# Optimization experiments

Measured on AMD Instinct MI355X. Metric: run time of the kernel, lower is better.

The kernel has to match this reference:

```python
import jax, jax.numpy as jnp
import numpy as np

NUM_HEADS = 8


def _forward(x, Wq, bq, Wk, bk, Wv, bv, Wo, bo, w1, b1, w2, b2, tau):
    B, S, E = x.shape
    H = NUM_HEADS
    hd = E // H
    scale = hd ** -0.5

    def heads(t):
        return t.reshape(B, S, H, hd).transpose(0, 2, 1, 3)  # [B,H,S,hd]

    q = heads(x @ Wq + bq)
    k = heads(x @ Wk + bk)
    v = heads(x @ Wv + bv)
    s = jnp.einsum('bhqd,bhkd->bhqk', q, k) * scale  # [B,H,S,S]

    # ---- autopoietic transform (vectorized over batch, no mask) ----
    s = jnp.clip(jnp.nan_to_num(s, nan=0.0, posinf=10.0, neginf=-10.0), -15.0, 15.0)
    ma = s.mean(axis=1)  # mean over heads -> [B,S,S]
    eps_safe = 0.05  # clamp(eps=1e-6, 0.05, 0.8)
    sa = jnp.clip(jnp.clip(ma, -8.0, 8.0) * eps_safe, -10.0, 10.0)
    # 1x1 conv on [1,1,S,S] == per-channel scalar scale+bias -> [B,C,S,S]
    hid = jax.nn.relu(jnp.clip(sa[:, None] * w1[None, :, None, None]
                               + b1[None, :, None, None], -5.0, 5.0))
    ap = jnp.clip(jnp.einsum('bcij,c->bij', hid, w2) + b2, -5.0, 5.0)
    taylor = jnp.clip(1.0 + 0.05 * (ap * 50.0), 0.5, 1.5)
    sig = jax.nn.sigmoid(taylor)
    p = jax.nn.softmax(jnp.clip(ma, -10.0, 10.0), axis=-1)
    Hent = -p * jnp.log(p + 1e-6)
    Fm = jax.nn.softmax(3.0 * Hent, axis=-1)
    t = sig * Fm
    eo = jnp.sqrt((ma * ma).sum(axis=(1, 2), keepdims=True)) + 1e-4  # fro norm
    et = jnp.sqrt((t * t).sum(axis=(1, 2), keepdims=True)) + 1e-4
    t = jnp.clip(eo / et, 0.8, 1.2) * t
    tm = t.mean(axis=(1, 2), keepdims=True)
    om = ma.mean(axis=(1, 2), keepdims=True)
    tstd = jnp.sqrt(jnp.clip(((t - tm) ** 2).mean(axis=(1, 2), keepdims=True), 0.01, None))
    ostd = jnp.sqrt(jnp.clip(((ma - om) ** 2).mean(axis=(1, 2), keepdims=True), 0.01, None))
    gd = jnp.clip(ostd / tstd, 0.8, 1.2)
    ar = jnp.clip(jnp.abs(ma).max(axis=(1, 2), keepdims=True), 1.0, 10.0)
    sm = jnp.clip(0.3 / jnp.log1p(ar), 0.1, 0.5)
    st = tm + sm * gd * (t - tm)  # scaled_transform
    ent = Hent.mean(axis=(1, 2), keepdims=True)
    ne = ent / jnp.log(jnp.float32(S))  # normalized entropy (max_entropy = log S)
    rr = 0.4 * (1.0 - jnp.clip(ne, 0.0, 0.4))  # residual ratio (base 0.4, entropy-damped)
    # blend transform back into per-head scores (res_scale = 1.0)
    s = s + rr[:, None] * (st - ma)[:, None]

    attn = jax.nn.softmax(s / tau, axis=-1)
    out = jnp.einsum('bhqk,bhkd->bhqd', attn, v)
    out = out.transpose(0, 2, 1, 3).reshape(B, S, E)
    return out @ Wo + bo


def setup_inputs() -> dict:
    key = jax.random.key(0)
    ks = jax.random.split(key, 8)
    B, S, E, C = 4, 512, 512, 128
    w_scale = 0.02
    return {
        'x': jax.random.normal(ks[0], (B, S, E), dtype=jnp.float32),
        'Wq': jax.random.normal(ks[1], (E, E), dtype=jnp.float32) * w_scale,
        'bq': jnp.zeros((E,), jnp.float32),
        'Wk': jax.random.normal(ks[2], (E, E), dtype=jnp.float32) * w_scale,
        'bk': jnp.zeros((E,), jnp.float32),
        'Wv': jax.random.normal(ks[3], (E, E), dtype=jnp.float32) * w_scale,
        'bv': jnp.zeros((E,), jnp.float32),
        'Wo': jax.random.normal(ks[4], (E, E), dtype=jnp.float32) * w_scale,
        'bo': jnp.zeros((E,), jnp.float32),
        'w1': jax.random.normal(ks[5], (C,), dtype=jnp.float32) * 0.5,
        'b1': jnp.zeros((C,), jnp.float32),
        'w2': jax.random.normal(ks[6], (C,), dtype=jnp.float32) * 0.1,
        'b2': jnp.zeros((1,), jnp.float32),
        'tau': jnp.ones((1,), jnp.float32),
    }


def reference(x, Wq, bq, Wk, bk, Wv, bv, Wo, bo, w1, b1, w2, b2, tau):
    return _forward(x, Wq, bq, Wk, bk, Wv, bv, Wo, bo, w1, b1, w2, b2, tau)
```

## Files before the change

### kernel.cpp

```cpp
#include <hip/hip_runtime.h>
#include <math.h>

#define BB 4
#define SS 512
#define EE 512
#define NH 8
#define HD 64
#define NC 128
#define NTAB 4096

typedef _Float16 f16x8 __attribute__((ext_vector_type(8)));
typedef float f32x4 __attribute__((ext_vector_type(4)));

struct HL { _Float16 h, l; };

__device__ __forceinline__ float clampf(float v, float lo, float hi) {
  return fminf(fmaxf(v, lo), hi);
}
__device__ __forceinline__ HL split16(float x) {
  HL r;
  r.h = (_Float16)x;
  r.l = (_Float16)(x - (float)r.h);
  return r;
}

__device__ __forceinline__ float waveRedSum(float v) {
#pragma unroll
  for (int o = 32; o; o >>= 1) v += __shfl_xor(v, o);
  return v;
}
__device__ __forceinline__ float waveRedMax(float v) {
#pragma unroll
  for (int o = 32; o; o >>= 1) v = fmaxf(v, __shfl_xor(v, o));
  return v;
}
__device__ __forceinline__ float blockRedSum(float v, float* red) {
  int tid = threadIdx.x;
  v = waveRedSum(v);
  __syncthreads();
  if ((tid & 63) == 0) red[tid >> 6] = v;
  __syncthreads();
  return red[0] + red[1] + red[2] + red[3];
}
__device__ __forceinline__ float blockRedMax(float v, float* red) {
  int tid = threadIdx.x;
  v = waveRedMax(v);
  __syncthreads();
  if ((tid & 63) == 0) red[tid >> 6] = v;
  __syncthreads();
  return fmaxf(fmaxf(red[0], red[1]), fmaxf(red[2], red[3]));
}

__global__ __launch_bounds__(256) void k_prep(
    const float* __restrict__ w1, const float* __restrict__ b1,
    const float* __restrict__ w2, const float* __restrict__ b2,
    float* __restrict__ T, const float* __restrict__ x,
    _Float16* __restrict__ xh, _Float16* __restrict__ xl,
    const float* __restrict__ Wq, const float* __restrict__ Wk,
    const float* __restrict__ Wv, const float* __restrict__ Wo,
    _Float16* __restrict__ Wth, _Float16* __restrict__ Wtl) {
  const int bid = blockIdx.x;
  const int tid = threadIdx.x;
  if (bid < 17) {
    int idx = bid * 256 + tid;
    if (idx > NTAB) return;
    float sa = -0.4f + (float)idx * (0.8f / (float)NTAB);
    float ap = 0.f;
#pragma unroll 4
    for (int c = 0; c < NC; ++c) {
      float h = fminf(fmaxf(sa * w1[c] + b1[c], 0.f), 5.f);
      ap += h * w2[c];
    }
    ap = clampf(ap + b2[0], -5.f, 5.f);
    float tay = clampf(1.0f + 0.05f * (ap * 50.0f), 0.5f, 1.5f);
    T[idx] = 1.0f / (1.0f + expf(-tay));
  } else if (bid < 529) {
    int idx = ((bid - 17) * 256 + tid) * 8;
    float4 u0 = *(const float4*)(x + idx);
    float4 u1 = *(const float4*)(x + idx + 4);
    float f[8] = {u0.x, u0.y, u0.z, u0.w, u1.x, u1.y, u1.z, u1.w};
    f16x8 h, l;
#pragma unroll
    for (int j = 0; j < 8; ++j) {
      HL r = split16(f[j]);
      h[j] = r.h;
      l[j] = r.l;
    }
    *(f16x8*)(xh + idx) = h;
    *(f16x8*)(xl + idx) = l;
  } else {
    const int j = bid - 529;
    const int z = j >> 6;
    const int rem = j & 63;
    const int k0 = (rem & 7) * 64, n0 = (rem >> 3) * 64;
    const float* W = (z == 0) ? Wq : (z == 1) ? Wk : (z == 2) ? Wv : Wo;
    __shared__ float Tt[64][68];
    const int r = tid >> 2, c = (tid & 3) * 16;
#pragma unroll
    for (int jj = 0; jj < 16; jj += 4)
      *(float4*)&Tt[r][c + jj] =
          *(const float4*)(W + (size_t)(k0 + r) * EE + n0 + c + jj);
    __syncthreads();
    f16x8 h0, l0, h1, l1;
#pragma unroll
    for (int jj = 0; jj < 8; ++jj) {
      HL r0 = split16(Tt[c + jj][r]);
      HL r1 = split16(Tt[c + 8 + jj][r]);
      h0[jj] = r0.h; l0[jj] = r0.l;
      h1[jj] = r1.h; l1[jj] = r1.l;
    }
    _Float16* dh = Wth + ((size_t)z * EE + n0 + r) * EE + k0 + c;
    _Float16* dl = Wtl + ((size_t)z * EE + n0 + r) * EE + k0 + c;
    *(f16x8*)dh = h0;
    *(f16x8*)(dh + 8) = h1;
    *(f16x8*)dl = l0;
    *(f16x8*)(dl + 8) = l1;
  }
}

__global__ __launch_bounds__(256) void k_qkv_mfma(
    const _Float16* __restrict__ xh, const _Float16* __restrict__ xl,
    const _Float16* __restrict__ Wth, const _Float16* __restrict__ Wtl,
    const float* __restrict__ bq, const float* __restrict__ bk,
    const float* __restrict__ bv,
    _Float16* __restrict__ qh, _Float16* __restrict__ ql,
    _Float16* __restrict__ kh, _Float16* __restrict__ kl,
    _Float16* __restrict__ vth, _Float16* __restrict__ vtl) {
  const int which = blockIdx.z;
  const int tid = threadIdx.x;
  const int wave = tid >> 6, lane = tid & 63;
  const int quad = lane >> 4, l16 = lane & 15;
  const int m0 = blockIdx.y * 64;
  const int n0 = blockIdx.x * 64;
  const _Float16* Bh = Wth + (size_t)which * EE * EE;
  const _Float16* Bl = Wtl + (size_t)which * EE * EE;

  __shared__ __align__(16) char smpool[36864];
  _Float16(*LAh)[72] = (_Float16(*)[72])(smpool);
  _Float16(*LAl)[72] = (_Float16(*)[72])(smpool + 9216);
  _Float16(*LBh)[72] = (_Float16(*)[72])(smpool + 18432);
  _Float16(*LBl)[72] = (_Float16(*)[72])(smpool + 27648);
  float(*TR)[68] = (float(*)[68])(smpool);

  const int sr0 = tid >> 3, sc0 = (tid & 7) * 8;
  const int sr1 = sr0 + 32;

  f16x8 rA0h = *(const f16x8*)(xh + (size_t)(m0 + sr0) * EE + sc0);
  f16x8 rA0l = *(const f16x8*)(xl + (size_t)(m0 + sr0) * EE + sc0);
  f16x8 rB0h = *(const f16x8*)(Bh + (size_t)(n0 + sr0) * EE + sc0);
  f16x8 rB0l = *(const f16x8*)(Bl + (size_t)(n0 + sr0) * EE + sc0);
  f16x8 rA1h = *(const f16x8*)(xh + (size_t)(m0 + sr1) * EE + sc0);
  f16x8 rA1l = *(const f16x8*)(xl + (size_t)(m0 + sr1) * EE + sc0);
  f16x8 rB1h = *(const f16x8*)(Bh + (size_t)(n0 + sr1) * EE + sc0);
  f16x8 rB1l = *(const f16x8*)(Bl + (size_t)(n0 + sr1) * EE + sc0);

  f32x4 acc[4] = {};
  for (int k0 = 0; k0 < EE; k0 += 64) {
    if (k0) __syncthreads();
    *(f16x8*)&LAh[sr0][sc0] = rA0h;
    *(f16x8*)&LAl[sr0][sc0] = rA0l;
    *(f16x8*)&LBh[sr0][sc0] = rB0h;
    *(f16x8*)&LBl[sr0][sc0] = rB0l;
    *(f16x8*)&LAh[sr1][sc0] = rA1h;
    *(f16x8*)&LAl[sr1][sc0] = rA1l;
    *(f16x8*)&LBh[sr1][sc0] = rB1h;
    *(f16x8*)&LBl[sr1][sc0] = rB1l;
    __syncthreads();
    if (k0 + 64 < EE) {
      const int kn = k0 + 64;
      rA0h = *(const f16x8*)(xh + (size_t)(m0 + sr0) * EE + kn + sc0);
      rA0l = *(const f16x8*)(xl + (size_t)(m0 + sr0) * EE + kn + sc0);
      rB0h = *(const f16x8*)(Bh + (size_t)(n0 + sr0) * EE + kn + sc0);
      rB0l = *(const f16x8*)(Bl + (size_t)(n0 + sr0) * EE + kn + sc0);
      rA1h = *(const f16x8*)(xh + (size_t)(m0 + sr1) * EE + kn + sc0);
      rA1l = *(const f16x8*)(xl + (size_t)(m0 + sr1) * EE + kn + sc0);
      rB1h = *(const f16x8*)(Bh + (size_t)(n0 + sr1) * EE + kn + sc0);
      rB1l = *(const f16x8*)(Bl + (size_t)(n0 + sr1) * EE + kn + sc0);
    }
#pragma unroll
    for (int kk = 0; kk < 64; kk += 32) {
      f16x8 ah = *(const f16x8*)&LAh[wave * 16 + l16][kk + quad * 8];
      f16x8 al = *(const f16x8*)&LAl[wave * 16 + l16][kk + quad * 8];
#pragma unroll
      for (int nt = 0; nt < 4; ++nt) {
        f16x8 bhf = *(const f16x8*)&LBh[nt * 16 + l16][kk + quad * 8];
        f16x8 blf = *(const f16x8*)&LBl[nt * 16 + l16][kk + quad * 8];
        acc[nt] = __builtin_amdgcn_mfma_f32_16x16x32_f16(ah, bhf, acc[nt], 0, 0, 0);
        acc[nt] = __builtin_amdgcn_mfma_f32_16x16x32_f16(ah, blf, acc[nt], 0, 0, 0);
        acc[nt] = __builtin_amdgcn_mfma_f32_16x16x32_f16(al, bhf, acc[nt], 0, 0, 0);
      }
    }
  }
  const float* bias = (which == 0) ? bq : (which == 1) ? bk : bv;
  if (which == 2) {
    __syncthreads();
#pragma unroll
    for (int nt = 0; nt < 4; ++nt) {
      const int dcol = nt * 16 + l16;
      const float bb = bias[n0 + nt * 16 + l16];
#pragma unroll
      for (int r = 0; r < 4; ++r)
        TR[dcol][wave * 16 + quad * 4 + r] = acc[nt][r] + bb;
    }
    __syncthreads();
    const int d = tid >> 2, cc = (tid & 3) * 16;
    const int bh = (m0 >> 9) * NH + (n0 >> 6);
    const int si0 = m0 & 511;
    f16x8 h0, l0, h1, l1;
#pragma unroll
    for (int jj = 0; jj < 8; ++jj) {
      HL r0 = split16(TR[d][cc + jj]);
      HL r1 = split16(TR[d][cc + 8 + jj]);
      h0[jj] = r0.h; l0[jj] = r0.l;
      h1[jj] = r1.h; l1[jj] = r1.l;
    }
    _Float16* dh = vth + ((size_t)bh * HD + d) * SS + si0 + cc;
    _Float16* dl = vtl + ((size_t)bh * HD + d) * SS + si0 + cc;
    *(f16x8*)dh = h0;
    *(f16x8*)(dh + 8) = h1;
    *(f16x8*)dl = l0;
    *(f16x8*)(dl + 8) = l1;
  } else {
    const float postscale = (which == 0) ? 0.125f : 1.0f;
    const int mbase = m0 + wave * 16 + quad * 4;
#pragma unroll
    for (int nt = 0; nt < 4; ++nt) {
      const int col = n0 + nt * 16 + l16;
      const float bb = bias[col];
      const int hh = col >> 6, d = col & 63;
#pragma unroll
      for (int r = 0; r < 4; ++r) {
        const int mm = mbase + r;
        const int b_ = mm >> 9, si = mm & 511;
        const size_t idx = (((size_t)(b_ * NH + hh)) * SS + si) * HD + d;
        const float val = (acc[nt][r] + bb) * postscale;
        HL sp = split16(val);
        (which ? kh : qh)[idx] = sp.h;
        (which ? kl : ql)[idx] = sp.l;
      }
    }
  }
}

__global__ __launch_bounds__(256) void k_scores_mfma(
    const _Float16* __restrict__ qh, const _Float16* __restrict__ ql,
    const _Float16* __restrict__ kh, const _Float16* __restrict__ kl,
    float* __restrict__ s) {
  const int bh = blockIdx.z;
  const int i0 = blockIdx.y * 64, j0 = blockIdx.x * 64;
  const int tid = threadIdx.x;
  const int wave = tid >> 6, lane = tid & 63;
  const int quad = lane >> 4, l16 = lane & 15;

  __shared__ _Float16 Qh[64][72], Ql[64][72], Kh[64][72], Kl[64][72];
  const int r = tid >> 2, c = (tid & 3) * 16;
  {
    const size_t qoff = ((size_t)bh * SS + i0 + r) * HD + c;
    const size_t koff = ((size_t)bh * SS + j0 + r) * HD + c;
    *(f16x8*)&Qh[r][c] = *(const f16x8*)(qh + qoff);
    *(f16x8*)&Qh[r][c + 8] = *(const f16x8*)(qh + qoff + 8);
    *(f16x8*)&Ql[r][c] = *(const f16x8*)(ql + qoff);
    *(f16x8*)&Ql[r][c + 8] = *(const f16x8*)(ql + qoff + 8);
    *(f16x8*)&Kh[r][c] = *(const f16x8*)(kh + koff);
    *(f16x8*)&Kh[r][c + 8] = *(const f16x8*)(kh + koff + 8);
    *(f16x8*)&Kl[r][c] = *(const f16x8*)(kl + koff);
    *(f16x8*)&Kl[r][c + 8] = *(const f16x8*)(kl + koff + 8);
  }
  __syncthreads();

  f16x8 a_hi[2], a_lo[2];
#pragma unroll
  for (int ks = 0; ks < 2; ++ks) {
    a_hi[ks] = *(const f16x8*)&Qh[wave * 16 + l16][ks * 32 + quad * 8];
    a_lo[ks] = *(const f16x8*)&Ql[wave * 16 + l16][ks * 32 + quad * 8];
  }
  f32x4 acc[4] = {};
#pragma unroll
  for (int ks = 0; ks < 2; ++ks) {
#pragma unroll
    for (int t = 0; t < 4; ++t) {
      f16x8 b_hi = *(const f16x8*)&Kh[t * 16 + l16][ks * 32 + quad * 8];
      f16x8 b_lo = *(const f16x8*)&Kl[t * 16 + l16][ks * 32 + quad * 8];
      acc[t] = __builtin_amdgcn_mfma_f32_16x16x32_f16(a_hi[ks], b_hi,
                                                      acc[t], 0, 0, 0);
      acc[t] = __builtin_amdgcn_mfma_f32_16x16x32_f16(a_hi[ks], b_lo,
                                                      acc[t], 0, 0, 0);
      acc[t] = __builtin_amdgcn_mfma_f32_16x16x32_f16(a_lo[ks], b_hi,
                                                      acc[t], 0, 0, 0);
    }
  }
  float* sb = s + (size_t)bh * SS * SS;
#pragma unroll
  for (int t = 0; t < 4; ++t) {
#pragma unroll
    for (int r2 = 0; r2 < 4; ++r2) {
      float val = clampf(acc[t][r2], -15.0f, 15.0f);
      sb[(size_t)(i0 + wave * 16 + quad * 4 + r2) * SS + j0 + t * 16 + l16] = val;
    }
  }
}

__global__ __launch_bounds__(64) void k_rowstat(
    const float* __restrict__ s, const float* __restrict__ T,
    float* __restrict__ ma, float* __restrict__ t_un,
    float* __restrict__ rowred) {
  const int row = blockIdx.x;
  const int b_ = row >> 9, i = row & 511;
  const int lane = threadIdx.x;

  float4 a0 = {0.f, 0.f, 0.f, 0.f}, a1 = {0.f, 0.f, 0.f, 0.f};
#pragma unroll
  for (int hh = 0; hh < NH; ++hh) {
    const float4* p = reinterpret_cast<const float4*>(
                          s + (((size_t)(b_ * NH + hh) * SS) + i) * SS) +
                      lane * 2;
    float4 u0 = p[0], u1 = p[1];
    a0.x += u0.x; a0.y += u0.y; a0.z += u0.z; a0.w += u0.w;
    a1.x += u1.x; a1.y += u1.y; a1.z += u1.z; a1.w += u1.w;
  }
  float m[8] = {a0.x * 0.125f, a0.y * 0.125f, a0.z * 0.125f, a0.w * 0.125f,
                a1.x * 0.125f, a1.y * 0.125f, a1.z * 0.125f, a1.w * 0.125f};
  {
    float4* mp = reinterpret_cast<float4*>(ma + ((size_t)b_ * SS + i) * SS) +
                 lane * 2;
    float4 w0 = {m[0], m[1], m[2], m[3]}, w1v = {m[4], m[5], m[6], m[7]};
    mp[0] = w0;
    mp[1] = w1v;
  }
  float sma = 0.f, sma2 = 0.f, mabs = 0.f;
#pragma unroll
  for (int e = 0; e < 8; ++e) {
    sma += m[e];
    sma2 += m[e] * m[e];
    mabs = fmaxf(mabs, fabsf(m[e]));
  }
  sma = waveRedSum(sma);
  sma2 = waveRedSum(sma2);
  mabs = waveRedMax(mabs);

  float ex[8], esum = 0.f;
#pragma unroll
  for (int e = 0; e < 8; ++e) {
    ex[e] = expf(clampf(m[e], -10.f, 10.f));
    esum += ex[e];
  }
  esum = waveRedSum(esum);
  float inv = 1.0f / esum;
  float Hv[8], sH = 0.f;
#pragma unroll
  for (int e = 0; e < 8; ++e) {
    float p = ex[e] * inv;
    Hv[e] = -p * logf(p + 1e-6f);
    sH += Hv[e];
  }
  sH = waveRedSum(sH);

  float fx[8], fsum = 0.f;
#pragma unroll
  for (int e = 0; e < 8; ++e) {
    fx[e] = expf(3.0f * Hv[e]);
    fsum += fx[e];
  }
  fsum = waveRedSum(fsum);
  float finv = 1.0f / fsum;

  float t[8], st = 0.f, st2 = 0.f;
#pragma unroll
  for (int e = 0; e < 8; ++e) {
    float sa = clampf(m[e], -8.f, 8.f) * 0.05f;
    float pos = (sa + 0.4f) * ((float)NTAB / 0.8f);
    int idx = (int)pos;
    idx = idx < 0 ? 0 : (idx > NTAB - 1 ? NTAB - 1 : idx);
    float frac = pos - (float)idx;
    float g0 = T[idx], g1 = T[idx + 1];
    float sig = g0 + (g1 - g0) * frac;
    t[e] = sig * fx[e] * finv;
    st += t[e];
    st2 += t[e] * t[e];
  }
  st = waveRedSum(st);
  st2 = waveRedSum(st2);
  {
    float4* tp = reinterpret_cast<float4*>(t_un + ((size_t)b_ * SS + i) * SS) +
                 lane * 2;
    float4 w0 = {t[0], t[1], t[2], t[3]}, w1v = {t[4], t[5], t[6], t[7]};
    tp[0] = w0;
    tp[1] = w1v;
  }
  if (lane == 0) {
    float* rp = rowred + (size_t)row * 8;
    rp[0] = sma; rp[1] = sma2; rp[2] = mabs;
    rp[3] = st;  rp[4] = st2;  rp[5] = sH;
  }
}

__global__ __launch_bounds__(256) void k_consts(
    const float* __restrict__ rowred, float* __restrict__ cst) {
  const int b_ = blockIdx.x;
  const int tid = threadIdx.x;
  __shared__ float red[4];
  const float* r0 = rowred + ((size_t)b_ * SS + tid * 2) * 8;
  const float* r1 = r0 + 8;
  float sma = blockRedSum(r0[0] + r1[0], red);
  float sma2 = blockRedSum(r0[1] + r1[1], red);
  float mabs = blockRedMax(fmaxf(r0[2], r1[2]), red);
  float st = blockRedSum(r0[3] + r1[3], red);
  float st2 = blockRedSum(r0[4] + r1[4], red);
  float sH = blockRedSum(r0[5] + r1[5], red);
  if (tid == 0) {
    const float N = (float)(SS * SS);
    float eo = sqrtf(sma2) + 1e-4f;
    float et = sqrtf(st2) + 1e-4f;
    float r = clampf(eo / et, 0.8f, 1.2f);
    float tmean = r * st / N;
    float om = sma / N;
    float vart = r * r * fmaxf(st2 / N - (st / N) * (st / N), 0.f);
    float tstd = sqrtf(fmaxf(vart, 0.01f));
    float varo = fmaxf(sma2 / N - om * om, 0.f);
    float ostd = sqrtf(fmaxf(varo, 0.01f));
    float gd = clampf(ostd / tstd, 0.8f, 1.2f);
    float ar = clampf(mabs, 1.f, 10.f);
    float sm = clampf(0.3f / log1pf(ar), 0.1f, 0.5f);
    float ent = sH / N;
    float ne = ent / logf((float)SS);
    float rr = 0.4f * (1.f - clampf(ne, 0.f, 0.4f));
    float G = sm * gd;
    cst[b_ * 4 + 0] = rr * (1.f - G) * tmean;
    cst[b_ * 4 + 1] = rr * G * r;
    cst[b_ * 4 + 2] = rr;
  }
}

__global__ __launch_bounds__(256) void k_av_fused(
    const float* __restrict__ s, const float* __restrict__ ma,
    const float* __restrict__ t_un, const float* __restrict__ cst,
    const float* __restrict__ tau, const _Float16* __restrict__ vth,
    const _Float16* __restrict__ vtl, _Float16* __restrict__ oh,
    _Float16* __restrict__ ol) {
  const int bh = blockIdx.y;
  const int b_ = bh >> 3, hh = bh & 7;
  const int m0 = blockIdx.x * 32;
  const int tid = threadIdx.x;
  const int wave = tid >> 6, lane = tid & 63;
  const int quad = lane >> 4, l16 = lane & 15;

  const float c0 = cst[b_ * 4 + 0], c1 = cst[b_ * 4 + 1], c2 = cst[b_ * 4 + 2];
  const float itau = 1.0f / tau[0];

  __shared__ _Float16 Ph[32][40], Pl[32][40];
  __shared__ float Zp[32][4];

  const bool stager = (tid < 128);
  const int srow = tid >> 2;
  const int ci = tid & 3;
  const int schunk = ci * 8;
  const size_t sbase = ((size_t)bh * SS + m0 + (srow & 31)) * SS + schunk;
  const size_t mbase = ((size_t)b_ * SS + m0 + (srow & 31)) * SS + schunk;

  float4 sv0, sv1, mv0, mv1, tv0, tv1;
  if (stager) {
    sv0 = *(const float4*)(s + sbase);
    sv1 = *(const float4*)(s + sbase + 4);
    mv0 = *(const float4*)(ma + mbase);
    mv1 = *(const float4*)(ma + mbase + 4);
    tv0 = *(const float4*)(t_un + mbase);
    tv1 = *(const float4*)(t_un + mbase + 4);
  }

  float zpart = 0.f;
  f32x4 acc[2] = {};
  for (int k0 = 0; k0 < SS; k0 += 32) {
    if (k0) __syncthreads();
    if (stager) {
      float svv[8] = {sv0.x, sv0.y, sv0.z, sv0.w, sv1.x, sv1.y, sv1.z, sv1.w};
      float mvv[8] = {mv0.x, mv0.y, mv0.z, mv0.w, mv1.x, mv1.y, mv1.z, mv1.w};
      float tvv[8] = {tv0.x, tv0.y, tv0.z, tv0.w, tv1.x, tv1.y, tv1.z, tv1.w};
      f16x8 hv, lv;
#pragma unroll
      for (int j = 0; j < 8; ++j) {
        float vv = (svv[j] + c0 + c1 * tvv[j] - c2 * mvv[j]) * itau;
        float e = expf(vv) * 1.52587890625e-05f;
        zpart += e;
        HL r = split16(e);
        hv[j] = r.h;
        lv[j] = r.l;
      }
      *(f16x8*)&Ph[srow][schunk] = hv;
      *(f16x8*)&Pl[srow][schunk] = lv;
    }
    __syncthreads();
    if (stager && k0 + 32 < SS) {
      sv0 = *(const float4*)(s + sbase + k0 + 32);
      sv1 = *(const float4*)(s + sbase + k0 + 36);
      mv0 = *(const float4*)(ma + mbase + k0 + 32);
      mv1 = *(const float4*)(ma + mbase + k0 + 36);
      tv0 = *(const float4*)(t_un + mbase + k0 + 32);
      tv1 = *(const float4*)(t_un + mbase + k0 + 36);
    }
    const size_t boff = ((size_t)bh * HD + wave * 16 + l16) * SS + k0 + quad * 8;
    f16x8 bh_ = *(const f16x8*)(vth + boff);
    f16x8 bl_ = *(const f16x8*)(vtl + boff);
#pragma unroll
    for (int mt = 0; mt < 2; ++mt) {
      f16x8 ah = *(const f16x8*)&Ph[mt * 16 + l16][quad * 8];
      f16x8 al = *(const f16x8*)&Pl[mt * 16 + l16][quad * 8];
      acc[mt] = __builtin_amdgcn_mfma_f32_16x16x32_f16(ah, bh_, acc[mt], 0, 0, 0);
      acc[mt] = __builtin_amdgcn_mfma_f32_16x16x32_f16(ah, bl_, acc[mt], 0, 0, 0);
      acc[mt] = __builtin_amdgcn_mfma_f32_16x16x32_f16(al, bh_, acc[mt], 0, 0, 0);
    }
  }
  __syncthreads();
  if (stager) Zp[srow][ci] = zpart;
  __syncthreads();
#pragma unroll
  for (int mt = 0; mt < 2; ++mt) {
#pragma unroll
    for (int r = 0; r < 4; ++r) {
      const int lr = mt * 16 + quad * 4 + r;
      const float Z = Zp[lr][0] + Zp[lr][1] + Zp[lr][2] + Zp[lr][3];
      const float oV = acc[mt][r] / Z;
      const int si = m0 + lr;
      const size_t idx =
          ((size_t)(b_ * SS + si)) * EE + hh * HD + wave * 16 + l16;
      HL sp = split16(oV);
      oh[idx] = sp.h;
      ol[idx] = sp.l;
    }
  }
}

__global__ __launch_bounds__(256) void k_out_mfma(
    const _Float16* __restrict__ oh, const _Float16* __restrict__ ol,
    const _Float16* __restrict__ Wth, const _Float16* __restrict__ Wtl,
    const float* __restrict__ bo, float* __restrict__ out) {
  const int tid = threadIdx.x;
  const int wave = tid >> 6, lane = tid & 63;
  const int quad = lane >> 4, l16 = lane & 15;
  const int m0 = blockIdx.y * 64;
  const int n0 = blockIdx.x * 64;
  const _Float16* Bh = Wth + (size_t)3 * EE * EE;
  const _Float16* Bl = Wtl + (size_t)3 * EE * EE;

  __shared__ _Float16 LAh[64][72], LAl[64][72], LBh[64][72], LBl[64][72];

  const int sr0 = tid >> 3, sc0 = (tid & 7) * 8;
  const int sr1 = sr0 + 32;

  f16x8 rA0h = *(const f16x8*)(oh + (size_t)(m0 + sr0) * EE + sc0);
  f16x8 rA0l = *(const f16x8*)(ol + (size_t)(m0 + sr0) * EE + sc0);
  f16x8 rB0h = *(const f16x8*)(Bh + (size_t)(n0 + sr0) * EE + sc0);
  f16x8 rB0l = *(const f16x8*)(Bl + (size_t)(n0 + sr0) * EE + sc0);
  f16x8 rA1h = *(const f16x8*)(oh + (size_t)(m0 + sr1) * EE + sc0);
  f16x8 rA1l = *(const f16x8*)(ol + (size_t)(m0 + sr1) * EE + sc0);
  f16x8 rB1h = *(const f16x8*)(Bh + (size_t)(n0 + sr1) * EE + sc0);
  f16x8 rB1l = *(const f16x8*)(Bl + (size_t)(n0 + sr1) * EE + sc0);

  f32x4 acc[4] = {};
  for (int k0 = 0; k0 < EE; k0 += 64) {
    if (k0) __syncthreads();
    *(f16x8*)&LAh[sr0][sc0] = rA0h;
    *(f16x8*)&LAl[sr0][sc0] = rA0l;
    *(f16x8*)&LBh[sr0][sc0] = rB0h;
    *(f16x8*)&LBl[sr0][sc0] = rB0l;
    *(f16x8*)&LAh[sr1][sc0] = rA1h;
    *(f16x8*)&LAl[sr1][sc0] = rA1l;
    *(f16x8*)&LBh[sr1][sc0] = rB1h;
    *(f16x8*)&LBl[sr1][sc0] = rB1l;
    __syncthreads();
    if (k0 + 64 < EE) {
      const int kn = k0 + 64;
      rA0h = *(const f16x8*)(oh + (size_t)(m0 + sr0) * EE + kn + sc0);
      rA0l = *(const f16x8*)(ol + (size_t)(m0 + sr0) * EE + kn + sc0);
      rB0h = *(const f16x8*)(Bh + (size_t)(n0 + sr0) * EE + kn + sc0);
      rB0l = *(const f16x8*)(Bl + (size_t)(n0 + sr0) * EE + kn + sc0);
      rA1h = *(const f16x8*)(oh + (size_t)(m0 + sr1) * EE + kn + sc0);
      rA1l = *(const f16x8*)(ol + (size_t)(m0 + sr1) * EE + kn + sc0);
      rB1h = *(const f16x8*)(Bh + (size_t)(n0 + sr1) * EE + kn + sc0);
      rB1l = *(const f16x8*)(Bl + (size_t)(n0 + sr1) * EE + kn + sc0);
    }
#pragma unroll
    for (int kk = 0; kk < 64; kk += 32) {
      f16x8 ah = *(const f16x8*)&LAh[wave * 16 + l16][kk + quad * 8];
      f16x8 al = *(const f16x8*)&LAl[wave * 16 + l16][kk + quad * 8];
#pragma unroll
      for (int nt = 0; nt < 4; ++nt) {
        f16x8 bhf = *(const f16x8*)&LBh[nt * 16 + l16][kk + quad * 8];
        f16x8 blf = *(const f16x8*)&LBl[nt * 16 + l16][kk + quad * 8];
        acc[nt] = __builtin_amdgcn_mfma_f32_16x16x32_f16(ah, bhf, acc[nt], 0, 0, 0);
        acc[nt] = __builtin_amdgcn_mfma_f32_16x16x32_f16(ah, blf, acc[nt], 0, 0, 0);
        acc[nt] = __builtin_amdgcn_mfma_f32_16x16x32_f16(al, bhf, acc[nt], 0, 0, 0);
      }
    }
  }
  const int mbase = m0 + wave * 16 + quad * 4;
#pragma unroll
  for (int nt = 0; nt < 4; ++nt) {
    const int col = n0 + nt * 16 + l16;
    const float bb = bo[col];
#pragma unroll
    for (int r = 0; r < 4; ++r) {
      const int m = mbase + r;
      out[(size_t)m * EE + col] = acc[nt][r] + bb;
    }
  }
}

extern "C" void kernel_launch(void* const* d_in, const int* in_sizes, int n_in,
                              void* d_out, int out_size, void* d_ws,
                              size_t ws_size, hipStream_t stream) {
  const float* x = (const float*)d_in[0];
  const float* Wq = (const float*)d_in[1];
  const float* bq = (const float*)d_in[2];
  const float* Wk = (const float*)d_in[3];
  const float* bk = (const float*)d_in[4];
  const float* Wv = (const float*)d_in[5];
  const float* bv = (const float*)d_in[6];
  const float* Wo = (const float*)d_in[7];
  const float* bo = (const float*)d_in[8];
  const float* w1 = (const float*)d_in[9];
  const float* b1 = (const float*)d_in[10];
  const float* w2 = (const float*)d_in[11];
  const float* b2 = (const float*)d_in[12];
  const float* tau = (const float*)d_in[13];
  float* out = (float*)d_out;

  const size_t NX = (size_t)2048 * EE;
  const size_t NW = (size_t)4 * EE * EE;
  const size_t NQK = (size_t)BB * NH * SS * HD;
  const size_t NS = (size_t)BB * NH * SS * SS;

  _Float16* xh = (_Float16*)d_ws;
  _Float16* xl = xh + NX;
  _Float16* Wth = xl + NX;
  _Float16* Wtl = Wth + NW;
  _Float16* qh = Wtl + NW;
  _Float16* ql = qh + NQK;
  _Float16* kh = ql + NQK;
  _Float16* kl = kh + NQK;
  _Float16* vth = kl + NQK;
  _Float16* vtl = vth + NQK;
  float* s = (float*)(vtl + NQK);
  float* ma = s + NS;
  float* t_un = ma + (size_t)BB * SS * SS;
  float* T = t_un + (size_t)BB * SS * SS;
  float* rowred = T + 8192;
  float* cst = rowred + 2048 * 8;
  _Float16* oh = xh;
  _Float16* ol = xl;

  k_prep<<<785, 256, 0, stream>>>(w1, b1, w2, b2, T, x, xh, xl, Wq, Wk, Wv, Wo,
                                  Wth, Wtl);
  k_qkv_mfma<<<dim3(8, 32, 3), 256, 0, stream>>>(xh, xl, Wth, Wtl, bq, bk, bv,
                                                 qh, ql, kh, kl, vth, vtl);
  k_scores_mfma<<<dim3(8, 8, 32), 256, 0, stream>>>(qh, ql, kh, kl, s);
  k_rowstat<<<2048, 64, 0, stream>>>(s, T, ma, t_un, rowred);
  k_consts<<<4, 256, 0, stream>>>(rowred, cst);
  k_av_fused<<<dim3(16, 32), 256, 0, stream>>>(s, ma, t_un, cst, tau, vth, vtl,
                                               oh, ol);
  k_out_mfma<<<dim3(8, 32), 256, 0, stream>>>(oh, ol, Wth, Wtl, bo, out);
}
```

Before: 167.4 us.

## Fuse x split into QKV GEMM and replace consts kernel with atomics

The QKV GEMM now reads fp32 x directly and splits it into high/low fp16 halves in registers, so the separate conversion pass and its workspace round trip are gone. Per-row statistics are accumulated per batch with global atomics, and every av block derives the constants itself, which removes the k_consts launch. k_rowstat packs four rows into each 256-thread block. The costs are redundant splitting of x across the N-tile blocks, atomic contention, and a float atomicMax done on the uint bit pattern, which is valid only because mabs is non-negative.

Measured after the change: 276.5 us. 65.1% more time.

```diff
diff --git a/kernel.cpp b/kernel.cpp
--- a/kernel.cpp
+++ b/kernel.cpp
@@ -34,31 +34,15 @@
   for (int o = 32; o; o >>= 1) v = fmaxf(v, __shfl_xor(v, o));
   return v;
 }
-__device__ __forceinline__ float blockRedSum(float v, float* red) {
-  int tid = threadIdx.x;
-  v = waveRedSum(v);
-  __syncthreads();
-  if ((tid & 63) == 0) red[tid >> 6] = v;
-  __syncthreads();
-  return red[0] + red[1] + red[2] + red[3];
-}
-__device__ __forceinline__ float blockRedMax(float v, float* red) {
-  int tid = threadIdx.x;
-  v = waveRedMax(v);
-  __syncthreads();
-  if ((tid & 63) == 0) red[tid >> 6] = v;
-  __syncthreads();
-  return fmaxf(fmaxf(red[0], red[1]), fmaxf(red[2], red[3]));
-}
 
 __global__ __launch_bounds__(256) void k_prep(
     const float* __restrict__ w1, const float* __restrict__ b1,
     const float* __restrict__ w2, const float* __restrict__ b2,
-    float* __restrict__ T, const float* __restrict__ x,
-    _Float16* __restrict__ xh, _Float16* __restrict__ xl,
+    float* __restrict__ T,
     const float* __restrict__ Wq, const float* __restrict__ Wk,
     const float* __restrict__ Wv, const float* __restrict__ Wo,
-    _Float16* __restrict__ Wth, _Float16* __restrict__ Wtl) {
+    _Float16* __restrict__ Wth, _Float16* __restrict__ Wtl,
+    float* __restrict__ acc) {
   const int bid = blockIdx.x;
   const int tid = threadIdx.x;
   if (bid < 17) {
@@ -74,22 +58,8 @@
     ap = clampf(ap + b2[0], -5.f, 5.f);
     float tay = clampf(1.0f + 0.05f * (ap * 50.0f), 0.5f, 1.5f);
     T[idx] = 1.0f / (1.0f + expf(-tay));
-  } else if (bid < 529) {
-    int idx = ((bid - 17) * 256 + tid) * 8;
-    float4 u0 = *(const float4*)(x + idx);
-    float4 u1 = *(const float4*)(x + idx + 4);
-    float f[8] = {u0.x, u0.y, u0.z, u0.w, u1.x, u1.y, u1.z, u1.w};
-    f16x8 h, l;
-#pragma unroll
-    for (int j = 0; j < 8; ++j) {
-      HL r = split16(f[j]);
-      h[j] = r.h;
-      l[j] = r.l;
-    }
-    *(f16x8*)(xh + idx) = h;
-    *(f16x8*)(xl + idx) = l;
-  } else {
-    const int j = bid - 529;
+  } else if (bid < 273) {
+    const int j = bid - 17;
     const int z = j >> 6;
     const int rem = j & 63;
     const int k0 = (rem & 7) * 64, n0 = (rem >> 3) * 64;
@@ -115,11 +85,13 @@
     *(f16x8*)(dh + 8) = h1;
     *(f16x8*)dl = l0;
     *(f16x8*)(dl + 8) = l1;
+  } else {
+    if (tid < 32) acc[tid] = 0.0f;
   }
 }
 
 __global__ __launch_bounds__(256) void k_qkv_mfma(
-    const _Float16* __restrict__ xh, const _Float16* __restrict__ xl,
+    const float* __restrict__ x,
     const _Float16* __restrict__ Wth, const _Float16* __restrict__ Wtl,
     const float* __restrict__ bq, const float* __restrict__ bk,
     const float* __restrict__ bv,
@@ -145,35 +117,49 @@
   const int sr0 = tid >> 3, sc0 = (tid & 7) * 8;
   const int sr1 = sr0 + 32;
 
-  f16x8 rA0h = *(const f16x8*)(xh + (size_t)(m0 + sr0) * EE + sc0);
-  f16x8 rA0l = *(const f16x8*)(xl + (size_t)(m0 + sr0) * EE + sc0);
+  float4 rx0a = *(const float4*)(x + (size_t)(m0 + sr0) * EE + sc0);
+  float4 rx0b = *(const float4*)(x + (size_t)(m0 + sr0) * EE + sc0 + 4);
+  float4 rx1a = *(const float4*)(x + (size_t)(m0 + sr1) * EE + sc0);
+  float4 rx1b = *(const float4*)(x + (size_t)(m0 + sr1) * EE + sc0 + 4);
   f16x8 rB0h = *(const f16x8*)(Bh + (size_t)(n0 + sr0) * EE + sc0);
   f16x8 rB0l = *(const f16x8*)(Bl + (size_t)(n0 + sr0) * EE + sc0);
-  f16x8 rA1h = *(const f16x8*)(xh + (size_t)(m0 + sr1) * EE + sc0);
-  f16x8 rA1l = *(const f16x8*)(xl + (size_t)(m0 + sr1) * EE + sc0);
   f16x8 rB1h = *(const f16x8*)(Bh + (size_t)(n0 + sr1) * EE + sc0);
   f16x8 rB1l = *(const f16x8*)(Bl + (size_t)(n0 + sr1) * EE + sc0);
 
   f32x4 acc[4] = {};
   for (int k0 = 0; k0 < EE; k0 += 64) {
     if (k0) __syncthreads();
-    *(f16x8*)&LAh[sr0][sc0] = rA0h;
-    *(f16x8*)&LAl[sr0][sc0] = rA0l;
+    {
+      float f0[8] = {rx0a.x, rx0a.y, rx0a.z, rx0a.w,
+                     rx0b.x, rx0b.y, rx0b.z, rx0b.w};
+      float f1[8] = {rx1a.x, rx1a.y, rx1a.z, rx1a.w,
+                     rx1b.x, rx1b.y, rx1b.z, rx1b.w};
+      f16x8 h0, l0, h1, l1;
+#pragma unroll
+      for (int j = 0; j < 8; ++j) {
+        HL r0 = split16(f0[j]);
+        HL r1 = split16(f1[j]);
+        h0[j] = r0.h; l0[j] = r0.l;
+        h1[j] = r1.h; l1[j] = r1.l;
+      }
+      *(f16x8*)&LAh[sr0][sc0] = h0;
+      *(f16x8*)&LAl[sr0][sc0] = l0;
+      *(f16x8*)&LAh[sr1][sc0] = h1;
+      *(f16x8*)&LAl[sr1][sc0] = l1;
+    }
     *(f16x8*)&LBh[sr0][sc0] = rB0h;
     *(f16x8*)&LBl[sr0][sc0] = rB0l;
-    *(f16x8*)&LAh[sr1][sc0] = rA1h;
-    *(f16x8*)&LAl[sr1][sc0] = rA1l;
     *(f16x8*)&LBh[sr1][sc0] = rB1h;
     *(f16x8*)&LBl[sr1][sc0] = rB1l;
     __syncthreads();
     if (k0 + 64 < EE) {
       const int kn = k0 + 64;
-      rA0h = *(const f16x8*)(xh + (size_t)(m0 + sr0) * EE + kn + sc0);
-      rA0l = *(const f16x8*)(xl + (size_t)(m0 + sr0) * EE + kn + sc0);
+      rx0a = *(const float4*)(x + (size_t)(m0 + sr0) * EE + kn + sc0);
+      rx0b = *(const float4*)(x + (size_t)(m0 + sr0) * EE + kn + sc0 + 4);
+      rx1a = *(const float4*)(x + (size_t)(m0 + sr1) * EE + kn + sc0);
+      rx1b = *(const float4*)(x + (size_t)(m0 + sr1) * EE + kn + sc0 + 4);
       rB0h = *(const f16x8*)(Bh + (size_t)(n0 + sr0) * EE + kn + sc0);
       rB0l = *(const f16x8*)(Bl + (size_t)(n0 + sr0) * EE + kn + sc0);
-      rA1h = *(const f16x8*)(xh + (size_t)(m0 + sr1) * EE + kn + sc0);
-      rA1l = *(const f16x8*)(xl + (size_t)(m0 + sr1) * EE + kn + sc0);
       rB1h = *(const f16x8*)(Bh + (size_t)(n0 + sr1) * EE + kn + sc0);
       rB1l = *(const f16x8*)(Bl + (size_t)(n0 + sr1) * EE + kn + sc0);
     }
@@ -300,13 +286,13 @@
   }
 }
 
-__global__ __launch_bounds__(64) void k_rowstat(
+__global__ __launch_bounds__(256) void k_rowstat(
     const float* __restrict__ s, const float* __restrict__ T,
     float* __restrict__ ma, float* __restrict__ t_un,
-    float* __restrict__ rowred) {
-  const int row = blockIdx.x;
+    float* __restrict__ acc) {
+  const int row = blockIdx.x * 4 + (threadIdx.x >> 6);
   const int b_ = row >> 9, i = row & 511;
-  const int lane = threadIdx.x;
+  const int lane = threadIdx.x & 63;
 
   float4 a0 = {0.f, 0.f, 0.f, 0.f}, a1 = {0.f, 0.f, 0.f, 0.f};
 #pragma unroll
@@ -388,27 +374,36 @@
     tp[1] = w1v;
   }
   if (lane == 0) {
-    float* rp = rowred + (size_t)row * 8;
-    rp[0] = sma; rp[1] = sma2; rp[2] = mabs;
-    rp[3] = st;  rp[4] = st2;  rp[5] = sH;
-  }
-}
-
-__global__ __launch_bounds__(256) void k_consts(
-    const float* __restrict__ rowred, float* __restrict__ cst) {
-  const int b_ = blockIdx.x;
+    float* ap = acc + b_ * 8;
+    atomicAdd(&ap[0], sma);
+    atomicAdd(&ap[1], sma2);
+    atomicMax((unsigned int*)&ap[2], __float_as_uint(mabs));
+    atomicAdd(&ap[3], st);
+    atomicAdd(&ap[4], st2);
+    atomicAdd(&ap[5], sH);
+  }
+}
+
+__global__ __launch_bounds__(256) void k_av_fused(
+    const float* __restrict__ s, const float* __restrict__ ma,
+    const float* __restrict__ t_un, const float* __restrict__ acc_g,
+    const float* __restrict__ tau, const _Float16* __restrict__ vth,
+    const _Float16* __restrict__ vtl, _Float16* __restrict__ oh,
+    _Float16* __restrict__ ol) {
+  const int bh = blockIdx.y;
+  const int b_ = bh >> 3, hh = bh & 7;
+  const int m0 = blockIdx.x * 32;
   const int tid = threadIdx.x;
-  __shared__ float red[4];
-  const float* r0 = rowred + ((size_t)b_ * SS + tid * 2) * 8;
-  const float* r1 = r0 + 8;
-  float sma = blockRedSum(r0[0] + r1[0], red);
-  float sma2 = blockRedSum(r0[1] + r1[1], red);
-  float mabs = blockRedMax(fmaxf(r0[2], r1[2]), red);
-  float st = blockRedSum(r0[3] + r1[3], red);
-  float st2 = blockRedSum(r0[4] + r1[4], red);
-  float sH = blockRedSum(r0[5] + r1[5], red);
-  if (tid == 0) {
+  const int wave = tid >> 6, lane = tid & 63;
+  const int quad = lane >> 4, l16 = lane & 15;
+
+  float c0, c1, c2;
+  {
+    const float* ap = acc_g + b_ * 8;
     const float N = (float)(SS * SS);
+    float sma = ap[0], sma2 = ap[1];
+    float mabs = __uint_as_float(((const unsigned int*)ap)[2]);
+    float st = ap[3], st2 = ap[4], sH = ap[5];
     float eo = sqrtf(sma2) + 1e-4f;
     float et = sqrtf(st2) + 1e-4f;
     float r = clampf(eo / et, 0.8f, 1.2f);
@@ -425,26 +420,10 @@
     float ne = ent / logf((float)SS);
     float rr = 0.4f * (1.f - clampf(ne, 0.f, 0.4f));
     float G = sm * gd;
-    cst[b_ * 4 + 0] = rr * (1.f - G) * tmean;
-    cst[b_ * 4 + 1] = rr * G * r;
-    cst[b_ * 4 + 2] = rr;
-  }
-}
-
-__global__ __launch_bounds__(256) void k_av_fused(
-    const float* __restrict__ s, const float* __restrict__ ma,
-    const float* __restrict__ t_un, const float* __restrict__ cst,
-    const float* __restrict__ tau, const _Float16* __restrict__ vth,
-    const _Float16* __restrict__ vtl, _Float16* __restrict__ oh,
-    _Float16* __restrict__ ol) {
-  const int bh = blockIdx.y;
-  const int b_ = bh >> 3, hh = bh & 7;
-  const int m0 = blockIdx.x * 32;
-  const int tid = threadIdx.x;
-  const int wave = tid >> 6, lane = tid & 63;
-  const int quad = lane >> 4, l16 = lane & 15;
-
-  const float c0 = cst[b_ * 4 + 0], c1 = cst[b_ * 4 + 1], c2 = cst[b_ * 4 + 2];
+    c0 = rr * (1.f - G) * tmean;
+    c1 = rr * G * r;
+    c2 = rr;
+  }
   const float itau = 1.0f / tau[0];
 
   __shared__ _Float16 Ph[32][40], Pl[32][40];
@@ -629,9 +608,7 @@
   const size_t NQK = (size_t)BB * NH * SS * HD;
   const size_t NS = (size_t)BB * NH * SS * SS;
 
-  _Float16* xh = (_Float16*)d_ws;
-  _Float16* xl = xh + NX;
-  _Float16* Wth = xl + NX;
+  _Float16* Wth = (_Float16*)d_ws;
   _Float16* Wtl = Wth + NW;
   _Float16* qh = Wtl + NW;
   _Float16* ql = qh + NQK;
@@ -639,23 +616,21 @@
   _Float16* kl = kh + NQK;
   _Float16* vth = kl + NQK;
   _Float16* vtl = vth + NQK;
-  float* s = (float*)(vtl + NQK);
+  _Float16* oh = vtl + NQK;
+  _Float16* ol = oh + NX;
+  float* s = (float*)(ol + NX);
   float* ma = s + NS;
   float* t_un = ma + (size_t)BB * SS * SS;
   float* T = t_un + (size_t)BB * SS * SS;
-  float* rowred = T + 8192;
-  float* cst = rowred + 2048 * 8;
-  _Float16* oh = xh;
-  _Float16* ol = xl;
-
-  k_prep<<<785, 256, 0, stream>>>(w1, b1, w2, b2, T, x, xh, xl, Wq, Wk, Wv, Wo,
-                                  Wth, Wtl);
-  k_qkv_mfma<<<dim3(8, 32, 3), 256, 0, stream>>>(xh, xl, Wth, Wtl, bq, bk, bv,
-                                                 qh, ql, kh, kl, vth, vtl);
+  float* acc = T + 8192;
+
+  k_prep<<<274, 256, 0, stream>>>(w1, b1, w2, b2, T, Wq, Wk, Wv, Wo, Wth, Wtl,
+                                  acc);
+  k_qkv_mfma<<<dim3(8, 32, 3), 256, 0, stream>>>(x, Wth, Wtl, bq, bk, bv, qh,
+                                                 ql, kh, kl, vth, vtl);
   k_scores_mfma<<<dim3(8, 8, 32), 256, 0, stream>>>(qh, ql, kh, kl, s);
-  k_rowstat<<<2048, 64, 0, stream>>>(s, T, ma, t_un, rowred);
-  k_consts<<<4, 256, 0, stream>>>(rowred, cst);
-  k_av_fused<<<dim3(16, 32), 256, 0, stream>>>(s, ma, t_un, cst, tau, vth, vtl,
+  k_rowstat<<<512, 256, 0, stream>>>(s, T, ma, t_un, acc);
+  k_av_fused<<<dim3(16, 32), 256, 0, stream>>>(s, ma, t_un, acc, tau, vth, vtl,
                                                oh, ol);
   k_out_mfma<<<dim3(8, 32), 256, 0, stream>>>(oh, ol, Wth, Wtl, bo, out);
 }
```
